# Optimization experiments

Measured on AMD Instinct MI355X. Metric: run time of the kernel, lower is better.

## Reference

```python
import jax, jax.numpy as jnp
import numpy as np

# ConvVAE2d config: img_size=64, kernel=stride=16 (same-padding -> 0 pad), non-overlapping patches
BS, CH, IMG, K, NC, HID, LAT = 1024, 3, 64, 16, 10, 1024, 128
OH = IMG // K          # patches per side = 4
L = OH * OH            # patches per image = 16
PD = CH * K * K        # flattened patch dim = 768


def setup_inputs() -> dict:
    key = jax.random.key(0)
    ks = jax.random.split(key, 8)
    def w(k_, shape, fan_in):
        return jax.random.normal(k_, shape, dtype=jnp.float32) * np.float32(1.0 / np.sqrt(fan_in))
    return {
        "x": jax.random.uniform(ks[0], (BS, CH, IMG, IMG), dtype=jnp.float32),
        "c": jax.random.uniform(ks[1], (BS, NC), dtype=jnp.float32),
        # cvae_small.encode params: [patch++class] -> hidden -> 2*latent
        "enc_w1": w(ks[2], (PD + NC, HID), PD + NC),
        "enc_b1": jnp.zeros((HID,), jnp.float32),
        "enc_w2": w(ks[3], (HID, 2 * LAT), HID),
        "enc_b2": jnp.zeros((2 * LAT,), jnp.float32),
        # cvae_small.decode params: [z++class] -> hidden -> patch (sigmoid)
        "dec_w1": w(ks[4], (LAT + NC, HID), LAT + NC),
        "dec_b1": jnp.zeros((HID,), jnp.float32),
        "dec_w2": w(ks[5], (HID, PD), HID),
        "dec_b2": jnp.zeros((PD,), jnp.float32),
    }


def reference(x, c, enc_w1, enc_b1, enc_w2, enc_b2, dec_w1, dec_b1, dec_w2, dec_b2):
    bs = x.shape[0]
    # --- encode_vae_layer: unfold into [bs, L, ch*k*k] patches (stride=k, pad=0) ---
    p = x.reshape(bs, CH, OH, K, OH, K).transpose(0, 2, 4, 1, 3, 5).reshape(bs, L, PD)
    cb = jnp.broadcast_to(c[:, None, :], (bs, L, NC))  # class vector per patch
    h = jax.nn.relu(jnp.concatenate([p, cb], axis=-1) @ enc_w1 + enc_b1)
    mu_logvar = h @ enc_w2 + enc_b2                    # [bs, L, 2*LAT]
    # --- reparameterize_vae_layer (deterministic=True -> z = mu) ---
    mu = mu_logvar[..., :LAT]
    # --- decode_vae_layer: per-patch decode, then fold back (non-overlapping) ---
    hd = jax.nn.relu(jnp.concatenate([mu, cb], axis=-1) @ dec_w1 + dec_b1)
    patches = jax.nn.sigmoid(hd @ dec_w2 + dec_b2)     # [bs, L, PD]
    recon = (patches.reshape(bs, OH, OH, CH, K, K)
                     .transpose(0, 3, 1, 4, 2, 5)
                     .reshape(bs, CH, IMG, IMG))
    # mu_logvar as a [bs, 2*latent, h/stride, w/stride] feature map
    mu_logvar_2d = mu_logvar.transpose(0, 2, 1).reshape(bs, 2 * LAT, OH, OH)
    return recon, mu_logvar_2d
```

## Files before the change

### kernel.cpp

```cpp
#include <hip/hip_runtime.h>

typedef unsigned short u16;
typedef unsigned int   u32;
typedef __bf16 bf16x8 __attribute__((ext_vector_type(8)));
typedef float  f32x4  __attribute__((ext_vector_type(4)));

__device__ __forceinline__ u16 f2b(float f) {
  u32 u = __builtin_bit_cast(u32, f);
  u = (u + 0x7fffu + ((u >> 16) & 1u)) >> 16;
  return (u16)u;
}
__device__ __forceinline__ float b2f(u16 h) {
  u32 u = ((u32)h) << 16;
  return __builtin_bit_cast(float, u);
}
__device__ __forceinline__ float ld_in(const void* p, size_t idx, int isf32) {
  return isf32 ? ((const float*)p)[idx] : b2f(((const u16*)p)[idx]);
}
__device__ __forceinline__ void async_cp16(const u16* g, u16* l) {
  __builtin_amdgcn_global_load_lds(
      (const __attribute__((address_space(1))) void*)g,
      (__attribute__((address_space(3))) void*)l, 16, 0, 0);
}

#define RECON_ELEMS 12582912
#define XB_STRIDE 12544

__global__ __launch_bounds__(256) void detect_f32(const u16* __restrict__ x,
                                                  int* __restrict__ flag) {
  __shared__ int s;
  if (threadIdx.x == 0) s = 0;
  __syncthreads();
  int bad = 0;
  for (int i = threadIdx.x; i < 2048; i += 256) {
    u16 u = x[i];
    if ((u & 0x8000u) || (u > 0x3F80u)) bad = 1;
  }
  if (bad) atomicOr(&s, 1);
  __syncthreads();
  if (threadIdx.x == 0) *flag = s;
}

__global__ __launch_bounds__(256) void prep_all(const void* __restrict__ x,
                                                const void* __restrict__ c,
                                                u16* __restrict__ xb,
                                                const void* __restrict__ ew1,
                                                const void* __restrict__ ew2,
                                                const void* __restrict__ dw1,
                                                const void* __restrict__ dw2,
                                                u16* __restrict__ W1t,
                                                u16* __restrict__ EW2t,
                                                u16* __restrict__ W3t,
                                                u16* __restrict__ DW2t,
                                                const int* __restrict__ flag) {
  __shared__ float t[32][33];
  const int blk = blockIdx.x;
  const int isf = *flag;
  if (blk < 6272) {
    const int g = blk * 256 + threadIdx.x;
    if (g < 1572864) {
      const size_t i = (size_t)g * 8;
      const int b = (int)(i / 12288);
      const int r = (int)(i - (size_t)b * 12288);
      u16* dst = xb + (size_t)b * XB_STRIDE + r;
      if (isf) {
        const float* s = (const float*)x + i;
        float4 f0 = *(const float4*)(s);
        float4 f1 = *(const float4*)(s + 4);
        dst[0] = f2b(f0.x); dst[1] = f2b(f0.y); dst[2] = f2b(f0.z); dst[3] = f2b(f0.w);
        dst[4] = f2b(f1.x); dst[5] = f2b(f1.y); dst[6] = f2b(f1.z); dst[7] = f2b(f1.w);
      } else {
        *(int4*)dst = *(const int4*)((const u16*)x + i);
      }
    } else if (g < 1605632) {
      const int t8 = g - 1572864;
      const int b = t8 >> 5;
      const int k8 = (t8 & 31) * 8;
      u16* dst = xb + (size_t)b * XB_STRIDE + 12288 + k8;
#pragma unroll
      for (int j = 0; j < 8; ++j) {
        const int col = k8 + j;
        dst[j] = (col < 10) ? f2b(ld_in(c, (size_t)b * 10 + col, isf)) : (u16)0;
      }
    }
    return;
  }
  const int pb = blk - 6272;
  const int z = pb >> 10;
  const int rem = pb & 1023;
  const int k0 = (rem & 31) * 32, n0 = (rem >> 5) * 32;
  const void* src; u16* dst; int N, Kpad, Ksrc;
  if (z == 0)      { src = ew1; dst = W1t;  N = 1024; Kpad = 800;  Ksrc = 778;  }
  else if (z == 1) { src = ew2; dst = EW2t; N = 256;  Kpad = 1024; Ksrc = 1024; }
  else if (z == 2) { src = dw1; dst = W3t;  N = 1024; Kpad = 160;  Ksrc = 138;  }
  else             { src = dw2; dst = DW2t; N = 768;  Kpad = 1024; Ksrc = 1024; }
  if (k0 >= Kpad || n0 >= N) return;
  const int tx = threadIdx.x & 31, ty = threadIdx.x >> 5;
#pragma unroll
  for (int j = 0; j < 4; ++j) {
    int k = k0 + ty + j * 8;
    t[ty + j * 8][tx] = (k < Ksrc) ? ld_in(src, (size_t)k * N + n0 + tx, isf) : 0.0f;
  }
  __syncthreads();
#pragma unroll
  for (int j = 0; j < 4; ++j) {
    int n = n0 + ty + j * 8;
    dst[(size_t)n * Kpad + k0 + tx] = f2b(t[tx][ty + j * 8]);
  }
}

template <int EPI, int AMODE>
__global__ __launch_bounds__(512, 2) void gemm_r3(const u16* __restrict__ A,
                                                  const u16* __restrict__ Bt,
                                                  const void* __restrict__ bias,
                                                  u16* __restrict__ outb,
                                                  float* __restrict__ outf,
                                                  int N, int K, int NBX, int NBY,
                                                  int rowOff,
                                                  const int* __restrict__ flag) {
  extern __shared__ __align__(16) u16 lds[];
  const int bid = blockIdx.x;
  const int xcd = bid & 7, idx = bid >> 3;
  const int byl = idx / NBX;
  const int by = xcd * (NBY >> 3) + byl;
  const int bx = idx - byl * NBX;
  const int rowBase = by * 256, colBase = bx * 256;

  const int tid = threadIdx.x;
  const int lane = tid & 63, w = tid >> 6;
  const int l16 = lane & 15, quad = lane >> 4;
  const int wm = w >> 2, wn = w & 3;
  const int swq = quad ^ ((l16 >> 1) & 3);

  const int isf = *flag;
  float bv[4];
#pragma unroll
  for (int nr = 0; nr < 4; ++nr)
    bv[nr] = ld_in(bias, colBase + wn * 64 + nr * 16 + l16, isf);
  asm volatile("s_waitcnt vmcnt(0)" ::: "memory");

  const int sA0 = tid, sA1 = tid + 512;
  const int rA0 = sA0 >> 2, qA0 = (sA0 & 3) ^ ((rA0 >> 1) & 3);
  const int rA1 = sA1 >> 2, qA1 = (sA1 & 3) ^ ((rA1 >> 1) & 3);
  const u16* gB0 = Bt + (size_t)(colBase + rA0) * K + qA0 * 8;
  const u16* gB1 = Bt + (size_t)(colBase + rA1) * K + qA1 * 8;
  const u16* gA0 = nullptr; const u16* gA1 = nullptr;
  int b1A0 = 0, b2A0 = 0, kq0 = 0, b1A1 = 0, b2A1 = 0, kq1 = 0;
  if (AMODE == 0) {
    gA0 = A + (size_t)(rowBase + rA0) * K + qA0 * 8;
    gA1 = A + (size_t)(rowBase + rA1) * K + qA1 * 8;
  } else {
    const int g0 = rowOff + rowBase + rA0, g1 = rowOff + rowBase + rA1;
    const int bb0 = g0 >> 4, ll0 = g0 & 15;
    const int bb1 = g1 >> 4, ll1 = g1 & 15;
    b1A0 = bb0 * XB_STRIDE + (ll0 >> 2) * 1024 + (ll0 & 3) * 16;
    b1A1 = bb1 * XB_STRIDE + (ll1 >> 2) * 1024 + (ll1 & 3) * 16;
    b2A0 = bb0 * XB_STRIDE + 11520;
    b2A1 = bb1 * XB_STRIDE + 11520;
    kq0 = qA0 * 8; kq1 = qA1 * 8;
  }
  auto aAddr = [&](int base1, int base2, int kq, int tt) -> const u16* {
    const int k = kq + (tt << 5);
    const int off = (k < 768)
        ? base1 + ((k >> 8) << 12) + (((k >> 4) & 15) << 6) + (k & 15)
        : base2 + k;
    return A + off;
  };
#define STAGE_T(tt, D) do {                                                \
    if (AMODE == 0) {                                                      \
      const int ko_ = (tt) * 32;                                           \
      async_cp16(gA0 + ko_, (D) + tid * 8);                                \
      async_cp16(gA1 + ko_, (D) + 4096 + tid * 8);                         \
    } else {                                                               \
      async_cp16(aAddr(b1A0, b2A0, kq0, (tt)), (D) + tid * 8);             \
      async_cp16(aAddr(b1A1, b2A1, kq1, (tt)), (D) + 4096 + tid * 8);      \
    }                                                                      \
    {                                                                      \
      const int ko_ = (tt) * 32;                                           \
      async_cp16(gB0 + ko_, (D) + 8192 + tid * 8);                         \
      async_cp16(gB1 + ko_, (D) + 12288 + tid * 8);                        \
    }                                                                      \
  } while (0)

  f32x4 acc[8][4] = {};
  bf16x8 a[8], b[4];
  const int NT = K >> 5;

  STAGE_T(0, lds);
  if (NT > 1) {
    STAGE_T(1, lds + 16384);
    asm volatile("s_waitcnt vmcnt(4)" ::: "memory");
  } else {
    asm volatile("s_waitcnt vmcnt(0)" ::: "memory");
  }
  __builtin_amdgcn_s_barrier();

  int cur = 0;
  for (int t = 0; t < NT; ++t) {
    const u16* Lq = lds + cur * 16384;
#pragma unroll
    for (int mr = 0; mr < 8; ++mr)
      a[mr] = *(const bf16x8*)(Lq + (wm * 128 + mr * 16 + l16) * 32 + swq * 8);
#pragma unroll
    for (int nr = 0; nr < 4; ++nr)
      b[nr] = *(const bf16x8*)(Lq + 8192 + (wn * 64 + nr * 16 + l16) * 32 + swq * 8);
    if (t + 2 < NT) {
      const int d2 = (cur >= 1) ? cur - 1 : 2;
      STAGE_T(t + 2, lds + d2 * 16384);
    }
    asm volatile("s_waitcnt lgkmcnt(0)" ::: "memory");
    __builtin_amdgcn_sched_barrier(0);
    __builtin_amdgcn_s_setprio(1);
#pragma unroll
    for (int mr = 0; mr < 8; ++mr)
#pragma unroll
      for (int nr = 0; nr < 4; ++nr)
        acc[mr][nr] = __builtin_amdgcn_mfma_f32_16x16x32_bf16(a[mr], b[nr], acc[mr][nr], 0, 0, 0);
    __builtin_amdgcn_s_setprio(0);
    __builtin_amdgcn_sched_barrier(0);
    if (t + 2 < NT)      asm volatile("s_waitcnt vmcnt(4)" ::: "memory");
    else if (t + 1 < NT) asm volatile("s_waitcnt vmcnt(0)" ::: "memory");
    if (t + 1 < NT) __builtin_amdgcn_s_barrier();
    cur = (cur >= 2) ? 0 : cur + 1;
  }
#undef STAGE_T

#pragma unroll
  for (int mr = 0; mr < 8; ++mr) {
    const int row0 = rowBase + wm * 128 + mr * 16 + quad * 4;
#pragma unroll
    for (int nr = 0; nr < 4; ++nr) {
      const int col = colBase + wn * 64 + nr * 16 + l16;
#pragma unroll
      for (int r = 0; r < 4; ++r) {
        const int row = row0 + r;
        float v = acc[mr][nr][r] + bv[nr];
        if (EPI == 0) {
          v = fmaxf(v, 0.0f);
          outb[(size_t)row * N + col] = f2b(v);
        } else {
          v = 1.0f / (1.0f + __expf(-v));
          const int grow = row + rowOff;
          const int bb = grow >> 4, l = grow & 15;
          const int oh = l >> 2, ow = l & 3;
          const int ch = col >> 8, kh = (col >> 4) & 15, kw = col & 15;
          outf[(size_t)bb * 12288 + ch * 4096 + (oh * 16 + kh) * 64 + ow * 16 + kw] = v;
        }
      }
    }
  }
}

__global__ __launch_bounds__(512, 2) void gemm_mid(u16* hio,
    const u16* __restrict__ EW2t, const u16* __restrict__ W3t,
    const void* __restrict__ c, const void* __restrict__ eb2,
    const void* __restrict__ db1, float* __restrict__ out2,
    int rowOff, const int* __restrict__ flag) {
  extern __shared__ __align__(16) u16 lds[];
  const int bid = blockIdx.x;
  const int lrowBase = bid * 64;
  const int growBase = rowOff + lrowBase;
  const int tid = threadIdx.x;
  const int lane = tid & 63, w = tid >> 6;
  const int l16 = lane & 15, quad = lane >> 4;
  const int swq = quad ^ ((l16 >> 1) & 3);
  const int wm = w >> 2, wn4 = w & 3;

  const int isf = *flag;
  float bv2[2], bv3[8][2];
#pragma unroll
  for (int nr = 0; nr < 2; ++nr)
    bv2[nr] = ld_in(eb2, w * 32 + nr * 16 + l16, isf);
#pragma unroll
  for (int np = 0; np < 8; ++np)
#pragma unroll
    for (int nr = 0; nr < 2; ++nr)
      bv3[np][nr] = ld_in(db1, np * 128 + wn4 * 32 + nr * 16 + l16, isf);
  asm volatile("s_waitcnt vmcnt(0)" ::: "memory");

  const int rA = tid >> 3, rcA = tid & 7;
  const int gcA = (rcA & 4) | ((rcA & 3) ^ ((rA >> 1) & 3));
  const u16* gAe = hio + (size_t)(lrowBase + rA) * 1024 + gcA * 8;
  const u16* gBe[4];
#pragma unroll
  for (int j = 0; j < 4; ++j) {
    const int sb = tid + j * 512;
    const int rB = sb >> 3, rcB = sb & 7;
    const int gcB = (rcB & 4) | ((rcB & 3) ^ ((rB >> 1) & 3));
    gBe[j] = EW2t + (size_t)rB * 1024 + gcB * 8;
  }

#define STGE(tt, s) do {                                                   \
    async_cp16(gAe + (tt) * 64, lds + (s) * 4096 + tid * 8);               \
    _Pragma("unroll") for (int j = 0; j < 4; ++j)                          \
      async_cp16(gBe[j] + (tt) * 64,                                       \
                 lds + 8192 + (s) * 16384 + (tid + j * 512) * 8);          \
  } while (0)

  f32x4 acce[4][2] = {};
  STGE(0, 0);
  int p = 0;
  for (int t = 0; t < 16; ++t) {
    if (t + 1 < 16) {
      STGE(t + 1, p ^ 1);
      asm volatile("s_waitcnt vmcnt(5)\n\ts_barrier" ::: "memory");
    } else {
      asm volatile("s_waitcnt vmcnt(0)\n\ts_barrier" ::: "memory");
    }
    const u16* AE = lds + p * 4096;
    const u16* BE = lds + 8192 + p * 16384;
    bf16x8 ae[4][2], be[2][2];
#pragma unroll
    for (int mr = 0; mr < 4; ++mr)
#pragma unroll
      for (int ks = 0; ks < 2; ++ks)
        ae[mr][ks] = *(const bf16x8*)(AE + (mr * 16 + l16) * 64 + ((ks * 4) | swq) * 8);
#pragma unroll
    for (int nr = 0; nr < 2; ++nr)
#pragma unroll
      for (int ks = 0; ks < 2; ++ks)
        be[nr][ks] = *(const bf16x8*)(BE + (w * 32 + nr * 16 + l16) * 64 + ((ks * 4) | swq) * 8);
    asm volatile("s_waitcnt lgkmcnt(0)" ::: "memory");
    __builtin_amdgcn_sched_barrier(0);
    __builtin_amdgcn_s_setprio(1);
#pragma unroll
    for (int mr = 0; mr < 4; ++mr)
#pragma unroll
      for (int nr = 0; nr < 2; ++nr)
#pragma unroll
        for (int ks = 0; ks < 2; ++ks)
          acce[mr][nr] = __builtin_amdgcn_mfma_f32_16x16x32_bf16(ae[mr][ks], be[nr][ks], acce[mr][nr], 0, 0, 0);
    __builtin_amdgcn_s_setprio(0);
    __builtin_amdgcn_sched_barrier(0);
    __builtin_amdgcn_s_barrier();
    p ^= 1;
  }
#undef STGE

  u16* A3 = lds + 40960;
#pragma unroll
  for (int mr = 0; mr < 4; ++mr)
#pragma unroll
    for (int nr = 0; nr < 2; ++nr) {
      const int col = w * 32 + nr * 16 + l16;
      const int row0 = mr * 16 + quad * 4;
#pragma unroll
      for (int r = 0; r < 4; ++r) {
        const int row = row0 + r;
        const int grow = growBase + row;
        const float v = acce[mr][nr][r] + bv2[nr];
        out2[(size_t)(grow >> 4) * 4096 + col * 16 + (grow & 15)] = v;
        if (col < 128) A3[row * 168 + col] = f2b(v);
      }
    }
  {
    const int rT = tid >> 3, cg = tid & 7;
    const int b = (growBase + rT) >> 4;
#pragma unroll
    for (int jj = 0; jj < 5; ++jj) {
      const int col = 128 + cg * 5 + jj;
      A3[rT * 168 + col] = (col < 138) ? f2b(ld_in(c, (size_t)b * 10 + col - 128, isf)) : (u16)0;
    }
  }
  asm volatile("s_waitcnt vmcnt(0) lgkmcnt(0)" ::: "memory");
  __builtin_amdgcn_s_barrier();

  int nW[5], cW[5];
#pragma unroll
  for (int j = 0; j < 5; ++j) {
    const int s5 = tid + j * 512;
    nW[j] = s5 / 20;
    cW[j] = s5 - nW[j] * 20;
  }
#pragma unroll
  for (int j = 0; j < 5; ++j)
    async_cp16(W3t + (size_t)nW[j] * 160 + cW[j] * 8, lds + (tid + j * 512) * 8);
  asm volatile("s_waitcnt vmcnt(0)" ::: "memory");
  __builtin_amdgcn_s_barrier();

  for (int np = 0; np < 8; ++np) {
    const int pb = np & 1;
    if (np < 7) {
#pragma unroll
      for (int j = 0; j < 5; ++j)
        async_cp16(W3t + (size_t)((np + 1) * 128 + nW[j]) * 160 + cW[j] * 8,
                   lds + (pb ^ 1) * 20480 + (tid + j * 512) * 8);
    }
    f32x4 accd[2][2] = {};
    const u16* WP = lds + pb * 20480;
#pragma unroll
    for (int t = 0; t < 5; ++t) {
      bf16x8 ad[2], bd[2];
#pragma unroll
      for (int mr = 0; mr < 2; ++mr)
        ad[mr] = *(const bf16x8*)(A3 + (wm * 32 + mr * 16 + l16) * 168 + (t * 4 + quad) * 8);
#pragma unroll
      for (int nr = 0; nr < 2; ++nr)
        bd[nr] = *(const bf16x8*)(WP + (wn4 * 32 + nr * 16 + l16) * 160 + (t * 4 + quad) * 8);
      asm volatile("s_waitcnt lgkmcnt(0)" ::: "memory");
      __builtin_amdgcn_sched_barrier(0);
#pragma unroll
      for (int mr = 0; mr < 2; ++mr)
#pragma unroll
        for (int nr = 0; nr < 2; ++nr)
          accd[mr][nr] = __builtin_amdgcn_mfma_f32_16x16x32_bf16(ad[mr], bd[nr], accd[mr][nr], 0, 0, 0);
    }
#pragma unroll
    for (int mr = 0; mr < 2; ++mr)
#pragma unroll
      for (int nr = 0; nr < 2; ++nr) {
        const int col = np * 128 + wn4 * 32 + nr * 16 + l16;
        const int row0 = wm * 32 + mr * 16 + quad * 4;
#pragma unroll
        for (int r = 0; r < 4; ++r) {
          const int row = row0 + r;
          const float v = fmaxf(accd[mr][nr][r] + bv3[np][nr], 0.0f);
          hio[(size_t)(lrowBase + row) * 1024 + col] = f2b(v);
        }
      }
    if (np < 7) {
      asm volatile("s_waitcnt vmcnt(16)" ::: "memory");
      __builtin_amdgcn_s_barrier();
    }
  }
}


extern "C" void kernel_launch(void* const* d_in, const int* in_sizes, int n_in,
                              void* d_out, int out_size, void* d_ws, size_t ws_size,
                              hipStream_t stream) {
  const void* x   = d_in[0];
  const void* c   = d_in[1];
  const void* ew1 = d_in[2];
  const void* eb1 = d_in[3];
  const void* ew2 = d_in[4];
  const void* eb2 = d_in[5];
  const void* dw1 = d_in[6];
  const void* db1 = d_in[7];
  const void* dw2 = d_in[8];
  const void* db2 = d_in[9];
  float* out  = (float*)d_out;
  u16*   ws   = (u16*)d_ws;

  static bool configured = false;
  if (!configured) {
    hipFuncSetAttribute(reinterpret_cast<const void*>(gemm_r3<0, 1>),
                        hipFuncAttributeMaxDynamicSharedMemorySize, 98304);
    hipFuncSetAttribute(reinterpret_cast<const void*>(gemm_r3<2, 0>),
                        hipFuncAttributeMaxDynamicSharedMemorySize, 98304);
    hipFuncSetAttribute(reinterpret_cast<const void*>(gemm_mid),
                        hipFuncAttributeMaxDynamicSharedMemorySize, 103424);
    configured = true;
  }

  const size_t fixedU16 = 8 + 819200 + 262144 + 163840 + 786432 + 12845056;
  int R = 2048;
  for (int cand = 16384; cand >= 2048; cand >>= 1) {
    if ((fixedU16 + (size_t)cand * 1024) * 2 <= ws_size) { R = cand; break; }
  }

  int* flag = (int*)ws;
  u16* W1t  = ws + 8;
  u16* EW2t = W1t + 819200;
  u16* W3t  = EW2t + 262144;
  u16* DW2t = W3t + 163840;
  u16* xb   = DW2t + 786432;
  u16* hc   = xb + 12845056;
  float* out2 = out + RECON_ELEMS;

  detect_f32<<<dim3(1), dim3(256), 0, stream>>>((const u16*)x, flag);

  prep_all<<<dim3(10368), dim3(256), 0, stream>>>(x, c, xb, ew1, ew2, dw1, dw2,
                                                  W1t, EW2t, W3t, DW2t, flag);

  const int chunks = 16384 / R;
  for (int chunk = 0; chunk < chunks; ++chunk) {
    int rowOff = chunk * R;
    const int NBY = R / 256;
    gemm_r3<0, 1><<<dim3(4 * NBY), dim3(512), 98304, stream>>>(xb, W1t, eb1, hc, nullptr,
                                                               1024, 800, 4, NBY, rowOff, flag);
    gemm_mid<<<dim3(R / 64), dim3(512), 103424, stream>>>(hc, EW2t, W3t, c, eb2, db1,
                                                          out2, rowOff, flag);
    gemm_r3<2, 0><<<dim3(3 * NBY), dim3(512), 98304, stream>>>(hc, DW2t, db2, nullptr, out,
                                                               768, 1024, 3, NBY, rowOff, flag);
  }
}
```

Before: 233.5 us.

## Switch GEMM to BK=64 double-buffered pipeline with split LDS reads

```diff
diff --git a/kernel.cpp b/kernel.cpp
--- a/kernel.cpp
+++ b/kernel.cpp
@@ -90,7 +90,7 @@
   const int rem = pb & 1023;
   const int k0 = (rem & 31) * 32, n0 = (rem >> 5) * 32;
   const void* src; u16* dst; int N, Kpad, Ksrc;
-  if (z == 0)      { src = ew1; dst = W1t;  N = 1024; Kpad = 800;  Ksrc = 778;  }
+  if (z == 0)      { src = ew1; dst = W1t;  N = 1024; Kpad = 832;  Ksrc = 778;  }
   else if (z == 1) { src = ew2; dst = EW2t; N = 256;  Kpad = 1024; Ksrc = 1024; }
   else if (z == 2) { src = dw1; dst = W3t;  N = 1024; Kpad = 160;  Ksrc = 138;  }
   else             { src = dw2; dst = DW2t; N = 768;  Kpad = 1024; Ksrc = 1024; }
@@ -110,7 +110,7 @@
 }
 
 template <int EPI, int AMODE>
-__global__ __launch_bounds__(512, 2) void gemm_r3(const u16* __restrict__ A,
+__global__ __launch_bounds__(512, 2) void gemm_r2(const u16* __restrict__ A,
                                                   const u16* __restrict__ Bt,
                                                   const void* __restrict__ bias,
                                                   u16* __restrict__ outb,
@@ -139,75 +139,76 @@
     bv[nr] = ld_in(bias, colBase + wn * 64 + nr * 16 + l16, isf);
   asm volatile("s_waitcnt vmcnt(0)" ::: "memory");
 
-  const int sA0 = tid, sA1 = tid + 512;
-  const int rA0 = sA0 >> 2, qA0 = (sA0 & 3) ^ ((rA0 >> 1) & 3);
-  const int rA1 = sA1 >> 2, qA1 = (sA1 & 3) ^ ((rA1 >> 1) & 3);
-  const u16* gB0 = Bt + (size_t)(colBase + rA0) * K + qA0 * 8;
-  const u16* gB1 = Bt + (size_t)(colBase + rA1) * K + qA1 * 8;
-  const u16* gA0 = nullptr; const u16* gA1 = nullptr;
-  int b1A0 = 0, b2A0 = 0, kq0 = 0, b1A1 = 0, b2A1 = 0, kq1 = 0;
+  const int rc = tid & 7;
+  int rowI[4], gcI[4];
+#pragma unroll
+  for (int i = 0; i < 4; ++i) {
+    rowI[i] = (tid >> 3) + i * 64;
+    gcI[i] = (rc & 4) | ((rc & 3) ^ ((rowI[i] >> 1) & 3));
+  }
+  const u16* gB[4];
+#pragma unroll
+  for (int i = 0; i < 4; ++i)
+    gB[i] = Bt + (size_t)(colBase + rowI[i]) * K + gcI[i] * 8;
+  const u16* gA[4] = {nullptr, nullptr, nullptr, nullptr};
+  int b1A[4], b2A[4], kqA[4];
+#pragma unroll
+  for (int i = 0; i < 4; ++i) { b1A[i] = 0; b2A[i] = 0; kqA[i] = 0; }
   if (AMODE == 0) {
-    gA0 = A + (size_t)(rowBase + rA0) * K + qA0 * 8;
-    gA1 = A + (size_t)(rowBase + rA1) * K + qA1 * 8;
+#pragma unroll
+    for (int i = 0; i < 4; ++i)
+      gA[i] = A + (size_t)(rowBase + rowI[i]) * K + gcI[i] * 8;
   } else {
-    const int g0 = rowOff + rowBase + rA0, g1 = rowOff + rowBase + rA1;
-    const int bb0 = g0 >> 4, ll0 = g0 & 15;
-    const int bb1 = g1 >> 4, ll1 = g1 & 15;
-    b1A0 = bb0 * XB_STRIDE + (ll0 >> 2) * 1024 + (ll0 & 3) * 16;
-    b1A1 = bb1 * XB_STRIDE + (ll1 >> 2) * 1024 + (ll1 & 3) * 16;
-    b2A0 = bb0 * XB_STRIDE + 11520;
-    b2A1 = bb1 * XB_STRIDE + 11520;
-    kq0 = qA0 * 8; kq1 = qA1 * 8;
-  }
-  auto aAddr = [&](int base1, int base2, int kq, int tt) -> const u16* {
-    const int k = kq + (tt << 5);
+#pragma unroll
+    for (int i = 0; i < 4; ++i) {
+      const int g0 = rowOff + rowBase + rowI[i];
+      const int bb = g0 >> 4, ll = g0 & 15;
+      b1A[i] = bb * XB_STRIDE + (ll >> 2) * 1024 + (ll & 3) * 16;
+      b2A[i] = bb * XB_STRIDE + 11520;
+      kqA[i] = gcI[i] * 8;
+    }
+  }
+  auto aAddr = [&](int i, int tt) -> const u16* {
+    const int k = kqA[i] + (tt << 6);
     const int off = (k < 768)
-        ? base1 + ((k >> 8) << 12) + (((k >> 4) & 15) << 6) + (k & 15)
-        : base2 + k;
+        ? b1A[i] + ((k >> 8) << 12) + (((k >> 4) & 15) << 6) + (k & 15)
+        : b2A[i] + k;
     return A + off;
   };
 #define STAGE_T(tt, D) do {                                                \
     if (AMODE == 0) {                                                      \
-      const int ko_ = (tt) * 32;                                           \
-      async_cp16(gA0 + ko_, (D) + tid * 8);                                \
-      async_cp16(gA1 + ko_, (D) + 4096 + tid * 8);                         \
+      const int ko_ = (tt) * 64;                                           \
+      _Pragma("unroll") for (int i = 0; i < 4; ++i)                        \
+        async_cp16(gA[i] + ko_, (D) + (tid + i * 512) * 8);                \
     } else {                                                               \
-      async_cp16(aAddr(b1A0, b2A0, kq0, (tt)), (D) + tid * 8);             \
-      async_cp16(aAddr(b1A1, b2A1, kq1, (tt)), (D) + 4096 + tid * 8);      \
+      _Pragma("unroll") for (int i = 0; i < 4; ++i)                        \
+        async_cp16(aAddr(i, (tt)), (D) + (tid + i * 512) * 8);             \
     }                                                                      \
     {                                                                      \
-      const int ko_ = (tt) * 32;                                           \
-      async_cp16(gB0 + ko_, (D) + 8192 + tid * 8);                         \
-      async_cp16(gB1 + ko_, (D) + 12288 + tid * 8);                        \
+      const int ko_ = (tt) * 64;                                           \
+      _Pragma("unroll") for (int i = 0; i < 4; ++i)                        \
+        async_cp16(gB[i] + ko_, (D) + 16384 + (tid + i * 512) * 8);        \
     }                                                                      \
   } while (0)
 
   f32x4 acc[8][4] = {};
   bf16x8 a[8], b[4];
-  const int NT = K >> 5;
+  const int NT = K >> 6;
 
   STAGE_T(0, lds);
-  if (NT > 1) {
-    STAGE_T(1, lds + 16384);
-    asm volatile("s_waitcnt vmcnt(4)" ::: "memory");
-  } else {
-    asm volatile("s_waitcnt vmcnt(0)" ::: "memory");
-  }
+  STAGE_T(1, lds + 32768);
+  asm volatile("s_waitcnt vmcnt(8)" ::: "memory");
   __builtin_amdgcn_s_barrier();
 
-  int cur = 0;
   for (int t = 0; t < NT; ++t) {
-    const u16* Lq = lds + cur * 16384;
+    const int p = t & 1;
+    const u16* Lq = lds + p * 32768;
 #pragma unroll
     for (int mr = 0; mr < 8; ++mr)
-      a[mr] = *(const bf16x8*)(Lq + (wm * 128 + mr * 16 + l16) * 32 + swq * 8);
+      a[mr] = *(const bf16x8*)(Lq + (wm * 128 + mr * 16 + l16) * 64 + swq * 8);
 #pragma unroll
     for (int nr = 0; nr < 4; ++nr)
-      b[nr] = *(const bf16x8*)(Lq + 8192 + (wn * 64 + nr * 16 + l16) * 32 + swq * 8);
-    if (t + 2 < NT) {
-      const int d2 = (cur >= 1) ? cur - 1 : 2;
-      STAGE_T(t + 2, lds + d2 * 16384);
-    }
+      b[nr] = *(const bf16x8*)(Lq + 16384 + (wn * 64 + nr * 16 + l16) * 64 + swq * 8);
     asm volatile("s_waitcnt lgkmcnt(0)" ::: "memory");
     __builtin_amdgcn_sched_barrier(0);
     __builtin_amdgcn_s_setprio(1);
@@ -218,10 +219,28 @@
         acc[mr][nr] = __builtin_amdgcn_mfma_f32_16x16x32_bf16(a[mr], b[nr], acc[mr][nr], 0, 0, 0);
     __builtin_amdgcn_s_setprio(0);
     __builtin_amdgcn_sched_barrier(0);
-    if (t + 2 < NT)      asm volatile("s_waitcnt vmcnt(4)" ::: "memory");
+#pragma unroll
+    for (int mr = 0; mr < 8; ++mr)
+      a[mr] = *(const bf16x8*)(Lq + (wm * 128 + mr * 16 + l16) * 64 + (4 | swq) * 8);
+#pragma unroll
+    for (int nr = 0; nr < 4; ++nr)
+      b[nr] = *(const bf16x8*)(Lq + 16384 + (wn * 64 + nr * 16 + l16) * 64 + (4 | swq) * 8);
+    asm volatile("s_waitcnt lgkmcnt(0)" ::: "memory");
+    __builtin_amdgcn_sched_barrier(0);
+    __builtin_amdgcn_s_barrier();
+    if (t + 2 < NT) STAGE_T(t + 2, lds + p * 32768);
+    __builtin_amdgcn_sched_barrier(0);
+    __builtin_amdgcn_s_setprio(1);
+#pragma unroll
+    for (int mr = 0; mr < 8; ++mr)
+#pragma unroll
+      for (int nr = 0; nr < 4; ++nr)
+        acc[mr][nr] = __builtin_amdgcn_mfma_f32_16x16x32_bf16(a[mr], b[nr], acc[mr][nr], 0, 0, 0);
+    __builtin_amdgcn_s_setprio(0);
+    __builtin_amdgcn_sched_barrier(0);
+    if (t + 2 < NT)      asm volatile("s_waitcnt vmcnt(8)" ::: "memory");
     else if (t + 1 < NT) asm volatile("s_waitcnt vmcnt(0)" ::: "memory");
     if (t + 1 < NT) __builtin_amdgcn_s_barrier();
-    cur = (cur >= 2) ? 0 : cur + 1;
   }
 #undef STAGE_T
 
@@ -444,16 +463,16 @@
 
   static bool configured = false;
   if (!configured) {
-    hipFuncSetAttribute(reinterpret_cast<const void*>(gemm_r3<0, 1>),
-                        hipFuncAttributeMaxDynamicSharedMemorySize, 98304);
-    hipFuncSetAttribute(reinterpret_cast<const void*>(gemm_r3<2, 0>),
-                        hipFuncAttributeMaxDynamicSharedMemorySize, 98304);
+    hipFuncSetAttribute(reinterpret_cast<const void*>(gemm_r2<0, 1>),
+                        hipFuncAttributeMaxDynamicSharedMemorySize, 131072);
+    hipFuncSetAttribute(reinterpret_cast<const void*>(gemm_r2<2, 0>),
+                        hipFuncAttributeMaxDynamicSharedMemorySize, 131072);
     hipFuncSetAttribute(reinterpret_cast<const void*>(gemm_mid),
                         hipFuncAttributeMaxDynamicSharedMemorySize, 103424);
     configured = true;
   }
 
-  const size_t fixedU16 = 8 + 819200 + 262144 + 163840 + 786432 + 12845056;
+  const size_t fixedU16 = 8 + 851968 + 262144 + 163840 + 786432 + 12845056;
   int R = 2048;
   for (int cand = 16384; cand >= 2048; cand >>= 1) {
     if ((fixedU16 + (size_t)cand * 1024) * 2 <= ws_size) { R = cand; break; }
@@ -461,7 +480,7 @@
 
   int* flag = (int*)ws;
   u16* W1t  = ws + 8;
-  u16* EW2t = W1t + 819200;
+  u16* EW2t = W1t + 851968;
   u16* W3t  = EW2t + 262144;
   u16* DW2t = W3t + 163840;
   u16* xb   = DW2t + 786432;
@@ -477,11 +496,11 @@
   for (int chunk = 0; chunk < chunks; ++chunk) {
     int rowOff = chunk * R;
     const int NBY = R / 256;
-    gemm_r3<0, 1><<<dim3(4 * NBY), dim3(512), 98304, stream>>>(xb, W1t, eb1, hc, nullptr,
-                                                               1024, 800, 4, NBY, rowOff, flag);
+    gemm_r2<0, 1><<<dim3(4 * NBY), dim3(512), 131072, stream>>>(xb, W1t, eb1, hc, nullptr,
+                                                                1024, 832, 4, NBY, rowOff, flag);
     gemm_mid<<<dim3(R / 64), dim3(512), 103424, stream>>>(hc, EW2t, W3t, c, eb2, db1,
                                                           out2, rowOff, flag);
-    gemm_r3<2, 0><<<dim3(3 * NBY), dim3(512), 98304, stream>>>(hc, DW2t, db2, nullptr, out,
-                                                               768, 1024, 3, NBY, rowOff, flag);
-  }
-}
+    gemm_r2<2, 0><<<dim3(3 * NBY), dim3(512), 131072, stream>>>(hc, DW2t, db2, nullptr, out,
+                                                                768, 1024, 3, NBY, rowOff, flag);
+  }
+}
```

New measurement: 240.5 us. 3.0% more time.
